# Performance work log

Measured on AMD Instinct MI355X. Metric: run time of the kernel, lower is better.

The kernel has to match this reference:

```python
import jax, jax.numpy as jnp
import numpy as np

EMBED_DIM = 1024
NUM_HEADS = 16
HEAD_DIM = EMBED_DIM // NUM_HEADS
ALPHA = 0.5  # mirror_bias['alpha'] default


def setup_inputs() -> dict:
    key = jax.random.key(0)
    k_x, k_m, kq, kk, kv, ko = jax.random.split(key, 6)
    B, S = 2, 2048
    x = jax.random.normal(k_x, (B, S, EMBED_DIM), dtype=jnp.float32)
    mask = jax.random.bernoulli(k_m, 0.1, (B, S))  # True = masked-out key (padding)
    # xavier_uniform for square [E,E]: limit = sqrt(6/(E+E))
    lim = float(np.sqrt(6.0 / (EMBED_DIM + EMBED_DIM)))
    Wq = jax.random.uniform(kq, (EMBED_DIM, EMBED_DIM), jnp.float32, -lim, lim)
    Wk = jax.random.uniform(kk, (EMBED_DIM, EMBED_DIM), jnp.float32, -lim, lim)
    Wv = jax.random.uniform(kv, (EMBED_DIM, EMBED_DIM), jnp.float32, -lim, lim)
    Wo = jax.random.uniform(ko, (EMBED_DIM, EMBED_DIM), jnp.float32, -lim, lim)
    return {"x": x, "Wq": Wq, "Wk": Wk, "Wv": Wv, "Wo": Wo, "mask": mask}


def _heads(t, B, S):
    # [B,S,E] -> [B,H,S,D]
    return t.reshape(B, S, NUM_HEADS, HEAD_DIM).transpose(0, 2, 1, 3)


def reference(x, Wq, Wk, Wv, Wo, mask):
    B, S, E = x.shape
    # nn.Linear(bias=False): y = x @ W.T
    q = _heads(x @ Wq.T, B, S)
    k = _heads(x @ Wk.T, B, S)
    v = _heads(x @ Wv.T, B, S)
    scores = jnp.einsum('bhqd,bhkd->bhqk', q, k) / jnp.sqrt(jnp.float32(HEAD_DIM))
    # mirror positional bias: target j = S-1-i
    i_idx = jnp.arange(S)[:, None]
    j_idx = jnp.arange(S)[None, :]
    dist = jnp.abs(j_idx - (S - 1 - i_idx)).astype(jnp.float32)
    bias = -ALPHA * (dist / jnp.float32(S))  # [S_q, S_k]
    scores = scores + bias[None, None, :, :]
    # bool 2D mask -> key padding mask [B,1,1,S_k], True = -inf
    scores = jnp.where(mask[:, None, None, :], -jnp.inf, scores)
    attn = jax.nn.softmax(scores, axis=-1)
    out = jnp.einsum('bhqk,bhkd->bhqd', attn, v)
    out = out.transpose(0, 2, 1, 3).reshape(B, S, E)
    return out @ Wo.T
```

## Files before the change

kernel.cpp:

```cpp
#include <hip/hip_runtime.h>

typedef unsigned short u16;
typedef unsigned int u32;
typedef unsigned long long u64;
typedef __attribute__((ext_vector_type(8))) short bf16x8;
typedef __attribute__((ext_vector_type(4))) float f32x4;
typedef __attribute__((ext_vector_type(2))) float f32x2;
typedef __attribute__((ext_vector_type(2))) unsigned int u32x2;
typedef __attribute__((ext_vector_type(4))) unsigned int u32x4;

#define MFMA16(A, B, C) __builtin_amdgcn_mfma_f32_16x16x32_bf16(A, B, C, 0, 0, 0)

__device__ __forceinline__ u16 f2bf(float f) {
  union { float f; unsigned u; } x; x.f = f;
  unsigned r = x.u + 0x7fffu + ((x.u >> 16) & 1u);
  return (u16)(r >> 16);
}

__device__ __forceinline__ u32 pack_bf2(float a, float b) {
  u32 r;
  asm("v_cvt_pk_bf16_f32 %0, %1, %2" : "=v"(r) : "v"(a), "v"(b));
  return r;
}

__device__ __forceinline__ f32x2 pk_fma(f32x2 a, f32x2 b, f32x2 c) {
  f32x2 d;
  asm("v_pk_fma_f32 %0, %1, %2, %3" : "=v"(d) : "v"(a), "v"(b), "v"(c));
  return d;
}
__device__ __forceinline__ f32x2 pk_add(f32x2 a, f32x2 b) {
  f32x2 d;
  asm("v_pk_add_f32 %0, %1, %2" : "=v"(d) : "v"(a), "v"(b));
  return d;
}

__device__ __forceinline__ void gload_lds16(const u16* g, u16* l) {
  __builtin_amdgcn_global_load_lds((const __attribute__((address_space(1))) void*)g,
                                   (__attribute__((address_space(3))) void*)l,
                                   16, 0, 0);
}

__global__ __launch_bounds__(256) void cvt_all(const float* __restrict__ x,
                                               const float* __restrict__ Wq,
                                               const float* __restrict__ Wk,
                                               const float* __restrict__ Wv,
                                               const float* __restrict__ Wo,
                                               const int* __restrict__ mask,
                                               u16* __restrict__ xb,
                                               u16* __restrict__ Wqkvb,
                                               u16* __restrict__ Wob,
                                               float* __restrict__ Mbg,
                                               int NE, int NW, int NB) {
  if ((int)blockIdx.x == NB) {
    const int t = threadIdx.x;
    const int j0 = t * 16;
    const float K3C = -8.0f * 1.44269504f;
    const float KMS = K3C - 1.0e6f;
#pragma unroll
    for (int jj = 0; jj < 16; jj += 4) {
      const int4 m4 = *(const int4*)(mask + j0 + jj);
      float4 o;
      o.x = m4.x ? KMS : K3C;
      o.y = m4.y ? KMS : K3C;
      o.z = m4.z ? KMS : K3C;
      o.w = m4.w ? KMS : K3C;
      *(float4*)(Mbg + j0 + jj) = o;
    }
    return;
  }
  const int e = (blockIdx.x * 256 + threadIdx.x) * 8;
  const float* s;
  u16* d;
  if (e < NE) { s = x + e; d = xb + e; }
  else {
    int f = e - NE;
    if (f < 3 * NW) {
      d = Wqkvb + f;
      s = (f < NW) ? Wq + f : (f < 2 * NW) ? Wk + (f - NW) : Wv + (f - 2 * NW);
    } else { f -= 3 * NW; s = Wo + f; d = Wob + f; }
  }
  const float4 a = *(const float4*)s;
  const float4 b = *(const float4*)(s + 4);
  bf16x8 o;
  o[0] = (short)f2bf(a.x); o[1] = (short)f2bf(a.y);
  o[2] = (short)f2bf(a.z); o[3] = (short)f2bf(a.w);
  o[4] = (short)f2bf(b.x); o[5] = (short)f2bf(b.y);
  o[6] = (short)f2bf(b.z); o[7] = (short)f2bf(b.w);
  *(bf16x8*)d = o;
}

__global__ __launch_bounds__(256) void gemm_qkv(const u16* __restrict__ A,
                                                const u16* __restrict__ B,
                                                u16* __restrict__ Qo,
                                                u16* __restrict__ Ko,
                                                u16* __restrict__ Vto,
                                                int M, int N, int K) {
  __shared__ alignas(16) u16 As[128 * 64];
  __shared__ alignas(16) u16 Bs[128 * 64];
  const int t = threadIdx.x;
  const int lane = t & 63, wave = t >> 6;
  const int quad = lane >> 4, l16 = lane & 15;
  const int bid = blockIdx.x;
  const int swz = (bid & 7) * 96 + (bid >> 3);
  const int m0 = (swz / 24) * 128, n0 = (swz % 24) * 128;
  const int wm = (wave >> 1) * 64, wn = (wave & 1) * 64;
  const int sx = l16 & 7;

  f32x4 acc[4][4] = {};

  for (int kk = 0; kk < K; kk += 64) {
#pragma unroll
    for (int i = 0; i < 4; i++) {
      const int c = t + i * 256;
      const int row = c >> 3, sub = c & 7;
      const int col = ((sub ^ (row & 7)) * 8);
      gload_lds16(A + (size_t)(m0 + row) * K + kk + col, As + (size_t)c * 8);
      gload_lds16(B + (size_t)(n0 + row) * K + kk + col, Bs + (size_t)c * 8);
    }
    __syncthreads();

#pragma unroll
    for (int ks = 0; ks < 2; ks++) {
      bf16x8 af[4], bfr[4];
#pragma unroll
      for (int i = 0; i < 4; i++)
        af[i] = *(const bf16x8*)(As + (wm + i * 16 + l16) * 64 +
                                 ((ks * 4 + quad) ^ sx) * 8);
#pragma unroll
      for (int j = 0; j < 4; j++)
        bfr[j] = *(const bf16x8*)(Bs + (wn + j * 16 + l16) * 64 +
                                  ((ks * 4 + quad) ^ sx) * 8);
#pragma unroll
      for (int i = 0; i < 4; i++)
#pragma unroll
        for (int j = 0; j < 4; j++)
          acc[i][j] = MFMA16(af[i], bfr[j], acc[i][j]);
    }
    __syncthreads();
  }

  const int G = ((m0 + wm) & 2047) >> 6;
#pragma unroll
  for (int j = 0; j < 4; j++) {
    const int col = n0 + wn + j * 16 + l16;
    if (col < 1024) {
#pragma unroll
      for (int i = 0; i < 4; i++)
#pragma unroll
        for (int r = 0; r < 4; r++)
          Qo[(size_t)(m0 + wm + i * 16 + quad * 4 + r) * 1024 + col] =
              f2bf(acc[i][j][r]);
    } else if (col < 2048) {
#pragma unroll
      for (int i = 0; i < 4; i++)
#pragma unroll
        for (int r = 0; r < 4; r++)
          Ko[(size_t)(m0 + wm + i * 16 + quad * 4 + r) * 1024 + (col - 1024)] =
              f2bf(acc[i][j][r]);
    } else {
      u16* base = Vto + ((size_t)(m0 >> 11) * 1024 + (col - 2048)) * 2048 + G * 64;
      const int C = 8 * (quad & 1) + 16 * (quad >> 1);
      u32x4 w0, w1;
      w0.x = pack_bf2(acc[0][j][0], acc[0][j][1]);
      w0.y = pack_bf2(acc[0][j][2], acc[0][j][3]);
      w0.z = pack_bf2(acc[1][j][0], acc[1][j][1]);
      w0.w = pack_bf2(acc[1][j][2], acc[1][j][3]);
      w1.x = pack_bf2(acc[2][j][0], acc[2][j][1]);
      w1.y = pack_bf2(acc[2][j][2], acc[2][j][3]);
      w1.z = pack_bf2(acc[3][j][0], acc[3][j][1]);
      w1.w = pack_bf2(acc[3][j][2], acc[3][j][3]);
      *(u32x4*)(base + C) = w0;
      *(u32x4*)(base + C + 32) = w1;
    }
  }
}

__global__ __launch_bounds__(256) void gemm_out(const u16* __restrict__ A,
                                                const u16* __restrict__ B,
                                                float* __restrict__ C,
                                                int M, int N, int K) {
  __shared__ alignas(16) u16 As[128 * 64];
  __shared__ alignas(16) u16 Bs[64 * 64];
  const int t = threadIdx.x;
  const int lane = t & 63, wave = t >> 6;
  const int quad = lane >> 4, l16 = lane & 15;
  const int bid = blockIdx.x;
  const int swz = (bid & 7) * 64 + (bid >> 3);
  const int m0 = (swz >> 4) * 128, n0 = (swz & 15) * 64;
  const int wm = (wave >> 1) * 64, wn = (wave & 1) * 32;
  const int sx = l16 & 7;

  f32x4 acc[4][2] = {};

  for (int kk = 0; kk < K; kk += 64) {
#pragma unroll
    for (int i = 0; i < 4; i++) {
      const int c = t + i * 256;
      const int row = c >> 3, sub = c & 7;
      gload_lds16(A + (size_t)(m0 + row) * K + kk + ((sub ^ (row & 7)) * 8),
                  As + (size_t)c * 8);
    }
#pragma unroll
    for (int i = 0; i < 2; i++) {
      const int c = t + i * 256;
      const int row = c >> 3, sub = c & 7;
      gload_lds16(B + (size_t)(n0 + row) * K + kk + ((sub ^ (row & 7)) * 8),
                  Bs + (size_t)c * 8);
    }
    __syncthreads();

#pragma unroll
    for (int ks = 0; ks < 2; ks++) {
      bf16x8 af[4], bfr[2];
#pragma unroll
      for (int i = 0; i < 4; i++)
        af[i] = *(const bf16x8*)(As + (wm + i * 16 + l16) * 64 +
                                 ((ks * 4 + quad) ^ sx) * 8);
#pragma unroll
      for (int j = 0; j < 2; j++)
        bfr[j] = *(const bf16x8*)(Bs + (wn + j * 16 + l16) * 64 +
                                  ((ks * 4 + quad) ^ sx) * 8);
#pragma unroll
      for (int i = 0; i < 4; i++)
#pragma unroll
        for (int j = 0; j < 2; j++)
          acc[i][j] = MFMA16(af[i], bfr[j], acc[i][j]);
    }
    __syncthreads();
  }

#pragma unroll
  for (int i = 0; i < 4; i++)
#pragma unroll
    for (int j = 0; j < 2; j++)
#pragma unroll
      for (int r = 0; r < 4; r++)
        C[(size_t)(m0 + wm + i * 16 + quad * 4 + r) * N + n0 + wn + j * 16 + l16] =
            acc[i][j][r];
}

__global__ __launch_bounds__(512) void attn_fwd(const u16* __restrict__ Q,
                                                const u16* __restrict__ Kb_,
                                                const u16* __restrict__ Vt,
                                                const float* __restrict__ Mb,
                                                u16* __restrict__ Ao) {
  constexpr int S = 2048, E = 1024;
  __shared__ alignas(16) u16 Ks[2][64 * 64];
  __shared__ alignas(16) u16 Vs[2][64 * 64];
  __shared__ alignas(16) float Msp[2048];
  __shared__ alignas(16) float Msm[2048];
  const int t = threadIdx.x;
  const int lane = t & 63, wave = t >> 6;
  const int quad = lane >> 4, l16 = lane & 15;
  const int bid = blockIdx.x;
  const int swz = (bid & 7) * 64 + (bid >> 3);
  const int xq = swz & 15, bh = swz >> 4;
  const int b = bh >> 4, h = bh & 15;
  const int q0 = xq * 128 + wave * 16;

  const int kr0 = t >> 3;
  const int kcol0 = ((t & 7) ^ (kr0 & 7)) * 8;
  const u16* kP0 = Kb_ + (size_t)(b * S + kr0) * E + h * 64 + kcol0;
  const u16* vbase = Vt + (size_t)(b * 16 + h) * 64 * S;
  const u16* vP0 = vbase + (size_t)kr0 * S + kcol0;

  bf16x8 aq[2];
  {
    const u16* qp = Q + ((size_t)(b * S) + q0 + l16) * E + h * 64;
    aq[0] = *(const bf16x8*)(qp + quad * 8);
    aq[1] = *(const bf16x8*)(qp + 32 + quad * 8);
  }

  const int sx = l16 & 7;
  const float K1 = 0.125f * 1.44269504f;
  const float K2 = 2.44140625e-4f * 1.44269504f;

  float lr = 0.f;
  f32x4 accO[4] = {};

  gload_lds16(kP0, Ks[0] + t * 8);
  gload_lds16(vP0, Vs[0] + t * 8);
  {
    const float4 m4 = *(const float4*)(Mb + b * 2048 + t * 4);
    const float kb = (float)(t * 4) - 2047.0f;
    float4 pp, mm;
    pp.x = fmaf(-K2, kb,       m4.x);  mm.x = fmaf(K2, kb,       m4.x);
    pp.y = fmaf(-K2, kb + 1.f, m4.y);  mm.y = fmaf(K2, kb + 1.f, m4.y);
    pp.z = fmaf(-K2, kb + 2.f, m4.z);  mm.z = fmaf(K2, kb + 2.f, m4.z);
    pp.w = fmaf(-K2, kb + 3.f, m4.w);  mm.w = fmaf(K2, kb + 3.f, m4.w);
    *(float4*)(Msp + t * 4) = pp;
    *(float4*)(Msm + t * 4) = mm;
  }
  __syncthreads();

  const float qn = (float)(q0 + l16);
  const float cqPs = -K2 * qn, cqMs = K2 * qn;
  const f32x2 K1p = {K1, K1};
  const f32x2 cqPp = {cqPs, cqPs}, cqMp = {cqMs, cqMs};
  const float fb0 = (float)(quad * 4 + q0 + l16 - 2047);
  const float twoK2 = 2.0f * K2;

  int buf = 0;
  for (int kc = 0; kc < 2048; kc += 64) {
    if (kc + 64 < 2048) {
      const int kn = kc + 64;
      gload_lds16(kP0 + (size_t)kn * E, Ks[buf ^ 1] + t * 8);
      gload_lds16(vP0 + kn, Vs[buf ^ 1] + t * 8);
    }
    const u16* ks = Ks[buf];
    const u16* vs = Vs[buf];

    bf16x8 bk[4][2];
#pragma unroll
    for (int T = 0; T < 4; T++)
#pragma unroll
      for (int dh = 0; dh < 2; dh++)
        bk[T][dh] = *(const bf16x8*)(ks + (T * 16 + l16) * 64 +
                                     ((dh * 4 + quad) ^ sx) * 8);

    f32x4 s[4] = {};
#pragma unroll
    for (int T = 0; T < 4; T++) {
      s[T] = MFMA16(bk[T][0], aq[0], s[T]);
      s[T] = MFMA16(bk[T][1], aq[1], s[T]);
    }

    const int kq = kc + q0;
    u32 pw[2][4];
    if (kq >= 2047 || kq <= 1969) {
      const float* mst = (kq >= 2047) ? Msp : Msm;
      const f32x2 cqp = (kq >= 2047) ? cqPp : cqMp;
#pragma unroll
      for (int T = 0; T < 4; T++) {
        const f32x4 m4v = *(const f32x4*)(mst + kc + 16 * T + quad * 4);
        const f32x2 s01 = {s[T][0], s[T][1]}, s23 = {s[T][2], s[T][3]};
        const f32x2 m01 = {m4v[0], m4v[1]}, m23 = {m4v[2], m4v[3]};
        const f32x2 a01 = pk_add(pk_fma(s01, K1p, m01), cqp);
        const f32x2 a23 = pk_add(pk_fma(s23, K1p, m23), cqp);
        const float p0 = __builtin_amdgcn_exp2f(a01[0]);
        const float p1 = __builtin_amdgcn_exp2f(a01[1]);
        const float p2 = __builtin_amdgcn_exp2f(a23[0]);
        const float p3 = __builtin_amdgcn_exp2f(a23[1]);
        lr += (p0 + p1) + (p2 + p3);
        pw[T >> 1][(T & 1) * 2 + 0] = pack_bf2(p0, p1);
        pw[T >> 1][(T & 1) * 2 + 1] = pack_bf2(p2, p3);
      }
    } else {
      const float fbLk = fb0 + (float)kc;
#pragma unroll
      for (int T = 0; T < 4; T++) {
        const f32x4 m4v = *(const f32x4*)(Msp + kc + 16 * T + quad * 4);
        float p[4];
#pragma unroll
        for (int r = 0; r < 4; r++) {
          const float fe = fbLk + (float)(16 * T + r);
          const float tv = fmaf(s[T][r], K1, m4v[r]) + cqPs;
          p[r] = __builtin_amdgcn_exp2f(fmaf(fminf(fe, 0.f), twoK2, tv));
        }
        lr += (p[0] + p[1]) + (p[2] + p[3]);
        pw[T >> 1][(T & 1) * 2 + 0] = pack_bf2(p[0], p[1]);
        pw[T >> 1][(T & 1) * 2 + 1] = pack_bf2(p[2], p[3]);
      }
    }

#pragma unroll
    for (int kst = 0; kst < 2; kst++) {
      bf16x8 bv[4];
#pragma unroll
      for (int tt = 0; tt < 4; tt++)
        bv[tt] = *(const bf16x8*)(vs + (tt * 16 + l16) * 64 +
                                  ((kst * 4 + quad) ^ sx) * 8);
      union { u32 w[4]; bf16x8 v; } ap;
      ap.w[0] = pw[kst][0]; ap.w[1] = pw[kst][1];
      ap.w[2] = pw[kst][2]; ap.w[3] = pw[kst][3];
#pragma unroll
      for (int tt = 0; tt < 4; tt++)
        accO[tt] = MFMA16(ap.v, bv[tt], accO[tt]);
    }

    __syncthreads();
    buf ^= 1;
  }

  u16* aob = Ao + ((size_t)(b * 2048 + q0)) * 1024 + h * 64;
  float l = lr;
  l += __shfl_xor(l, 16);
  l += __shfl_xor(l, 32);
  float linv[4];
#pragma unroll
  for (int r = 0; r < 4; r++) linv[r] = 1.0f / __shfl(l, quad * 4 + r);
#pragma unroll
  for (int r = 0; r < 4; r++) {
    u16* arow = aob + (size_t)(quad * 4 + r) * 1024;
#pragma unroll
    for (int tt = 0; tt < 4; tt++)
      arow[tt * 16 + l16] = f2bf(accO[tt][r] * linv[r]);
  }
}

extern "C" void kernel_launch(void* const* d_in, const int* in_sizes, int n_in,
                              void* d_out, int out_size, void* d_ws, size_t ws_size,
                              hipStream_t stream) {
  const float* x  = (const float*)d_in[0];
  const float* Wq = (const float*)d_in[1];
  const float* Wk = (const float*)d_in[2];
  const float* Wv = (const float*)d_in[3];
  const float* Wo = (const float*)d_in[4];
  const int* mask = (const int*)d_in[5];

  const int M = 4096, N = 1024, K = 1024;
  const int NE = M * N, NW = N * K;
  const int NB = (NE + 4 * NW) / 2048;

  u16* xb    = (u16*)d_ws;
  u16* Wqkvb = xb + NE;
  u16* Wob   = Wqkvb + (size_t)3 * NW;
  u16* Qb    = Wob + NW;
  u16* Kb    = Qb + NE;
  u16* Vt    = Kb + NE;
  u16* Ao    = Vt + NE;
  float* Mbg = (float*)(Ao + NE);

  cvt_all<<<NB + 1, 256, 0, stream>>>(x, Wq, Wk, Wv, Wo, mask,
                                      xb, Wqkvb, Wob, Mbg, NE, NW, NB);

  gemm_qkv<<<768, 256, 0, stream>>>(xb, Wqkvb, Qb, Kb, Vt, M, 3072, K);
  attn_fwd<<<512, 512, 0, stream>>>(Qb, Kb, Vt, Mbg, Ao);
  gemm_out<<<512, 256, 0, stream>>>(Ao, Wob, (float*)d_out, M, N, K);
}
```

Before: 185.8 us.

## Split key range across wave halves with two query tiles per wave

Each wave now handles 32 queries (two 16-row tiles) over half of the key sequence. The block loads both key halves per iteration into doubled LDS buffers, and the two halves' partial outputs and row sums are merged through shared memory at the end. This reuses each K/V fragment read from LDS for two query tiles and halves the loop trip count. In exchange it doubles LDS use, raises register pressure, and adds a final reduction step. The no-mask branch threshold is adjusted to match the 32-row query tiles.

```diff
diff --git a/kernel.cpp b/kernel.cpp
--- a/kernel.cpp
+++ b/kernel.cpp
@@ -245,41 +245,47 @@
                                                 const float* __restrict__ Mb,
                                                 u16* __restrict__ Ao) {
   constexpr int S = 2048, E = 1024;
-  __shared__ alignas(16) u16 Ks[2][64 * 64];
-  __shared__ alignas(16) u16 Vs[2][64 * 64];
+  __shared__ alignas(16) u16 Ks[2][2][64 * 64];
+  __shared__ alignas(16) u16 Vs[2][2][64 * 64];
   __shared__ alignas(16) float Msp[2048];
   __shared__ alignas(16) float Msm[2048];
   const int t = threadIdx.x;
   const int lane = t & 63, wave = t >> 6;
   const int quad = lane >> 4, l16 = lane & 15;
+  const int qg = wave & 3, kh = wave >> 2;
   const int bid = blockIdx.x;
   const int swz = (bid & 7) * 64 + (bid >> 3);
   const int xq = swz & 15, bh = swz >> 4;
   const int b = bh >> 4, h = bh & 15;
-  const int q0 = xq * 128 + wave * 16;
+  const int q0 = xq * 128 + qg * 32;
 
   const int kr0 = t >> 3;
   const int kcol0 = ((t & 7) ^ (kr0 & 7)) * 8;
-  const u16* kP0 = Kb_ + (size_t)(b * S + kr0) * E + h * 64 + kcol0;
+  const u16* kPh0 = Kb_ + (size_t)(b * S + kr0) * E + h * 64 + kcol0;
+  const u16* kPh1 = Kb_ + (size_t)(b * S + 1024 + kr0) * E + h * 64 + kcol0;
   const u16* vbase = Vt + (size_t)(b * 16 + h) * 64 * S;
-  const u16* vP0 = vbase + (size_t)kr0 * S + kcol0;
-
-  bf16x8 aq[2];
-  {
-    const u16* qp = Q + ((size_t)(b * S) + q0 + l16) * E + h * 64;
-    aq[0] = *(const bf16x8*)(qp + quad * 8);
-    aq[1] = *(const bf16x8*)(qp + 32 + quad * 8);
+  const u16* vPh0 = vbase + (size_t)kr0 * S + kcol0;
+  const u16* vPh1 = vbase + (size_t)kr0 * S + 1024 + kcol0;
+
+  bf16x8 aq[2][2];
+#pragma unroll
+  for (int qt = 0; qt < 2; qt++) {
+    const u16* qp = Q + ((size_t)(b * S) + q0 + qt * 16 + l16) * E + h * 64;
+    aq[qt][0] = *(const bf16x8*)(qp + quad * 8);
+    aq[qt][1] = *(const bf16x8*)(qp + 32 + quad * 8);
   }
 
   const int sx = l16 & 7;
   const float K1 = 0.125f * 1.44269504f;
   const float K2 = 2.44140625e-4f * 1.44269504f;
 
-  float lr = 0.f;
-  f32x4 accO[4] = {};
-
-  gload_lds16(kP0, Ks[0] + t * 8);
-  gload_lds16(vP0, Vs[0] + t * 8);
+  float lr[2] = {};
+  f32x4 accO[2][4] = {};
+
+  gload_lds16(kPh0, Ks[0][0] + t * 8);
+  gload_lds16(kPh1, Ks[0][1] + t * 8);
+  gload_lds16(vPh0, Vs[0][0] + t * 8);
+  gload_lds16(vPh1, Vs[0][1] + t * 8);
   {
     const float4 m4 = *(const float4*)(Mb + b * 2048 + t * 4);
     const float kb = (float)(t * 4) - 2047.0f;
@@ -293,22 +299,25 @@
   }
   __syncthreads();
 
-  const float qn = (float)(q0 + l16);
-  const float cqPs = -K2 * qn, cqMs = K2 * qn;
+  const float qn0 = (float)(q0 + l16), qn1 = (float)(q0 + 16 + l16);
   const f32x2 K1p = {K1, K1};
-  const f32x2 cqPp = {cqPs, cqPs}, cqMp = {cqMs, cqMs};
-  const float fb0 = (float)(quad * 4 + q0 + l16 - 2047);
+  const float cqPs[2] = {-K2 * qn0, -K2 * qn1};
+  const float cqMs[2] = {K2 * qn0, K2 * qn1};
   const float twoK2 = 2.0f * K2;
+  const int kbase = kh * 1024;
 
   int buf = 0;
-  for (int kc = 0; kc < 2048; kc += 64) {
-    if (kc + 64 < 2048) {
+  for (int kc = 0; kc < 1024; kc += 64) {
+    if (kc + 64 < 1024) {
       const int kn = kc + 64;
-      gload_lds16(kP0 + (size_t)kn * E, Ks[buf ^ 1] + t * 8);
-      gload_lds16(vP0 + kn, Vs[buf ^ 1] + t * 8);
-    }
-    const u16* ks = Ks[buf];
-    const u16* vs = Vs[buf];
+      gload_lds16(kPh0 + (size_t)kn * E, Ks[buf ^ 1][0] + t * 8);
+      gload_lds16(kPh1 + (size_t)kn * E, Ks[buf ^ 1][1] + t * 8);
+      gload_lds16(vPh0 + kn, Vs[buf ^ 1][0] + t * 8);
+      gload_lds16(vPh1 + kn, Vs[buf ^ 1][1] + t * 8);
+    }
+    const u16* ks = Ks[buf][kh];
+    const u16* vs = Vs[buf][kh];
+    const int kabs = kbase + kc;
 
     bf16x8 bk[4][2];
 #pragma unroll
@@ -318,48 +327,59 @@
         bk[T][dh] = *(const bf16x8*)(ks + (T * 16 + l16) * 64 +
                                      ((dh * 4 + quad) ^ sx) * 8);
 
-    f32x4 s[4] = {};
-#pragma unroll
-    for (int T = 0; T < 4; T++) {
-      s[T] = MFMA16(bk[T][0], aq[0], s[T]);
-      s[T] = MFMA16(bk[T][1], aq[1], s[T]);
-    }
-
-    const int kq = kc + q0;
-    u32 pw[2][4];
-    if (kq >= 2047 || kq <= 1969) {
+    f32x4 s[2][4] = {};
+#pragma unroll
+    for (int qt = 0; qt < 2; qt++)
+#pragma unroll
+      for (int T = 0; T < 4; T++) {
+        s[qt][T] = MFMA16(bk[T][0], aq[qt][0], s[qt][T]);
+        s[qt][T] = MFMA16(bk[T][1], aq[qt][1], s[qt][T]);
+      }
+
+    const int kq = kabs + q0;
+    u32 pw[2][2][4];
+    if (kq >= 2047 || kq <= 1953) {
       const float* mst = (kq >= 2047) ? Msp : Msm;
-      const f32x2 cqp = (kq >= 2047) ? cqPp : cqMp;
+      const float* cqs = (kq >= 2047) ? cqPs : cqMs;
 #pragma unroll
       for (int T = 0; T < 4; T++) {
-        const f32x4 m4v = *(const f32x4*)(mst + kc + 16 * T + quad * 4);
-        const f32x2 s01 = {s[T][0], s[T][1]}, s23 = {s[T][2], s[T][3]};
+        const f32x4 m4v = *(const f32x4*)(mst + kabs + 16 * T + quad * 4);
         const f32x2 m01 = {m4v[0], m4v[1]}, m23 = {m4v[2], m4v[3]};
-        const f32x2 a01 = pk_add(pk_fma(s01, K1p, m01), cqp);
-        const f32x2 a23 = pk_add(pk_fma(s23, K1p, m23), cqp);
-        const float p0 = __builtin_amdgcn_exp2f(a01[0]);
-        const float p1 = __builtin_amdgcn_exp2f(a01[1]);
-        const float p2 = __builtin_amdgcn_exp2f(a23[0]);
-        const float p3 = __builtin_amdgcn_exp2f(a23[1]);
-        lr += (p0 + p1) + (p2 + p3);
-        pw[T >> 1][(T & 1) * 2 + 0] = pack_bf2(p0, p1);
-        pw[T >> 1][(T & 1) * 2 + 1] = pack_bf2(p2, p3);
+#pragma unroll
+        for (int qt = 0; qt < 2; qt++) {
+          const f32x2 cqp = {cqs[qt], cqs[qt]};
+          const f32x2 s01 = {s[qt][T][0], s[qt][T][1]};
+          const f32x2 s23 = {s[qt][T][2], s[qt][T][3]};
+          const f32x2 a01 = pk_add(pk_fma(s01, K1p, m01), cqp);
+          const f32x2 a23 = pk_add(pk_fma(s23, K1p, m23), cqp);
+          const float p0 = __builtin_amdgcn_exp2f(a01[0]);
+          const float p1 = __builtin_amdgcn_exp2f(a01[1]);
+          const float p2 = __builtin_amdgcn_exp2f(a23[0]);
+          const float p3 = __builtin_amdgcn_exp2f(a23[1]);
+          lr[qt] += (p0 + p1) + (p2 + p3);
+          pw[qt][T >> 1][(T & 1) * 2 + 0] = pack_bf2(p0, p1);
+          pw[qt][T >> 1][(T & 1) * 2 + 1] = pack_bf2(p2, p3);
+        }
       }
     } else {
-      const float fbLk = fb0 + (float)kc;
 #pragma unroll
       for (int T = 0; T < 4; T++) {
-        const f32x4 m4v = *(const f32x4*)(Msp + kc + 16 * T + quad * 4);
-        float p[4];
-#pragma unroll
-        for (int r = 0; r < 4; r++) {
-          const float fe = fbLk + (float)(16 * T + r);
-          const float tv = fmaf(s[T][r], K1, m4v[r]) + cqPs;
-          p[r] = __builtin_amdgcn_exp2f(fmaf(fminf(fe, 0.f), twoK2, tv));
+        const f32x4 m4v = *(const f32x4*)(Msp + kabs + 16 * T + quad * 4);
+#pragma unroll
+        for (int qt = 0; qt < 2; qt++) {
+          const float fbLk =
+              (float)(quad * 4 + q0 + qt * 16 + l16 - 2047 + kabs + 16 * T);
+          float p[4];
+#pragma unroll
+          for (int r = 0; r < 4; r++) {
+            const float fe = fbLk + (float)r;
+            const float tv = fmaf(s[qt][T][r], K1, m4v[r]) + cqPs[qt];
+            p[r] = __builtin_amdgcn_exp2f(fmaf(fminf(fe, 0.f), twoK2, tv));
+          }
+          lr[qt] += (p[0] + p[1]) + (p[2] + p[3]);
+          pw[qt][T >> 1][(T & 1) * 2 + 0] = pack_bf2(p[0], p[1]);
+          pw[qt][T >> 1][(T & 1) * 2 + 1] = pack_bf2(p[2], p[3]);
         }
-        lr += (p[0] + p[1]) + (p[2] + p[3]);
-        pw[T >> 1][(T & 1) * 2 + 0] = pack_bf2(p[0], p[1]);
-        pw[T >> 1][(T & 1) * 2 + 1] = pack_bf2(p[2], p[3]);
       }
     }
 
@@ -370,31 +390,63 @@
       for (int tt = 0; tt < 4; tt++)
         bv[tt] = *(const bf16x8*)(vs + (tt * 16 + l16) * 64 +
                                   ((kst * 4 + quad) ^ sx) * 8);
-      union { u32 w[4]; bf16x8 v; } ap;
-      ap.w[0] = pw[kst][0]; ap.w[1] = pw[kst][1];
-      ap.w[2] = pw[kst][2]; ap.w[3] = pw[kst][3];
-#pragma unroll
-      for (int tt = 0; tt < 4; tt++)
-        accO[tt] = MFMA16(ap.v, bv[tt], accO[tt]);
+#pragma unroll
+      for (int qt = 0; qt < 2; qt++) {
+        union { u32 w[4]; bf16x8 v; } ap;
+        ap.w[0] = pw[qt][kst][0]; ap.w[1] = pw[qt][kst][1];
+        ap.w[2] = pw[qt][kst][2]; ap.w[3] = pw[qt][kst][3];
+#pragma unroll
+        for (int tt = 0; tt < 4; tt++)
+          accO[qt][tt] = MFMA16(ap.v, bv[tt], accO[qt][tt]);
+      }
     }
 
     __syncthreads();
     buf ^= 1;
   }
 
+  float* scrA = (float*)Ks;
+  float* scrL = (float*)Vs;
+  const int sidx = qg * 64 + lane;
+  if (kh == 1) {
+#pragma unroll
+    for (int qt = 0; qt < 2; qt++) {
+#pragma unroll
+      for (int tt = 0; tt < 4; tt++)
+        *(f32x4*)(scrA + sidx * 32 + (qt * 4 + tt) * 4) = accO[qt][tt];
+      scrL[sidx * 2 + qt] = lr[qt];
+    }
+  }
+  __syncthreads();
+  if (kh == 1) return;
+
+#pragma unroll
+  for (int qt = 0; qt < 2; qt++) {
+#pragma unroll
+    for (int tt = 0; tt < 4; tt++) {
+      const f32x4 o = *(const f32x4*)(scrA + sidx * 32 + (qt * 4 + tt) * 4);
+      accO[qt][tt][0] += o[0]; accO[qt][tt][1] += o[1];
+      accO[qt][tt][2] += o[2]; accO[qt][tt][3] += o[3];
+    }
+    lr[qt] += scrL[sidx * 2 + qt];
+  }
+
   u16* aob = Ao + ((size_t)(b * 2048 + q0)) * 1024 + h * 64;
-  float l = lr;
-  l += __shfl_xor(l, 16);
-  l += __shfl_xor(l, 32);
-  float linv[4];
-#pragma unroll
-  for (int r = 0; r < 4; r++) linv[r] = 1.0f / __shfl(l, quad * 4 + r);
-#pragma unroll
-  for (int r = 0; r < 4; r++) {
-    u16* arow = aob + (size_t)(quad * 4 + r) * 1024;
-#pragma unroll
-    for (int tt = 0; tt < 4; tt++)
-      arow[tt * 16 + l16] = f2bf(accO[tt][r] * linv[r]);
+#pragma unroll
+  for (int qt = 0; qt < 2; qt++) {
+    float l = lr[qt];
+    l += __shfl_xor(l, 16);
+    l += __shfl_xor(l, 32);
+    float linv[4];
+#pragma unroll
+    for (int r = 0; r < 4; r++) linv[r] = 1.0f / __shfl(l, quad * 4 + r);
+#pragma unroll
+    for (int r = 0; r < 4; r++) {
+      u16* arow = aob + (size_t)(qt * 16 + quad * 4 + r) * 1024;
+#pragma unroll
+      for (int tt = 0; tt < 4; tt++)
+        arow[tt * 16 + l16] = f2bf(accO[qt][tt][r] * linv[r]);
+    }
   }
 }
 
```

After: 192.4 us. 1.04x slower.
